# Optimization experiments

Hardware: AMD Instinct MI355X
Metric: run time of the kernel (lower is better)

## Reference

```python
import jax, jax.numpy as jnp
import numpy as np

B, T, R = 512, 4096, 16


def setup_inputs() -> dict:
    key = jax.random.key(0)
    k1, k2, k3 = jax.random.split(key, 3)
    pred = jax.random.normal(k1, (B, T, R), dtype=jnp.float32)
    target = jax.random.normal(k2, (B, T, R), dtype=jnp.float32)
    # replicate_mask marks a contiguous prefix of valid replicates (matches
    # the original `pred[b, :, :n_valid]` slicing). Lengths in [0, R].
    lengths = jax.random.randint(k3, (B,), 0, R + 1)
    replicate_mask = (jnp.arange(R)[None, :] < lengths[:, None]).astype(jnp.float32)
    return {"pred": pred, "target": target, "replicate_mask": replicate_mask}


def _masked_var_unbiased(x, m, n_safe):
    # x: [B,T,R], m: [B,1,R], n_safe: [B,1] (clamped >= 2)
    mean = jnp.sum(x * m, axis=-1, keepdims=True) / n_safe[:, :, None]  # [B,T,1]
    sq = jnp.sum(((x - mean) ** 2) * m, axis=-1)  # [B,T]
    return sq / (n_safe - 1.0)  # unbiased (torch var default ddof=1)


def reference(pred, target, replicate_mask):
    weight = 0.1
    n = jnp.sum(replicate_mask, axis=-1)  # [B]
    n_safe = jnp.maximum(n, 2.0)[:, None]  # avoid div-by-zero; masked out below
    m = replicate_mask[:, None, :]  # [B,1,R]
    pred_var = _masked_var_unbiased(pred, m, n_safe)      # [B,T]
    target_var = _masked_var_unbiased(target, m, n_safe)  # [B,T]
    mse = jnp.mean((pred_var - target_var) ** 2, axis=-1)  # [B]
    valid = n > 1.0
    n_multi = jnp.sum(valid.astype(jnp.float32))
    total = jnp.sum(jnp.where(valid, mse, 0.0))
    loss = jnp.where(n_multi > 0, total / jnp.maximum(n_multi, 1.0), 0.0)
    return weight * loss
```

## Files before the change

### kernel.cpp

```cpp
#include <hip/hip_runtime.h>

#define B_DIM 512
#define T_DIM 4096
#define NSLOT 256
#define BLOCKS 16384
#define THREADS 256
#define NWAVE (THREADS / 64)
#define ITER 2

__device__ __forceinline__ float hsum4(float4 v) { return (v.x + v.y) + (v.z + v.w); }

__device__ __forceinline__ float mdot(float4 x, float4 m) {
    return (x.x * m.x + x.y * m.y) + (x.z * m.z + x.w * m.w);
}

__device__ __forceinline__ float mdot2(float4 x, float4 m) {
    return (x.x * x.x * m.x + x.y * x.y * m.y) + (x.z * x.z * m.z + x.w * x.w * m.w);
}

__device__ __forceinline__ float qsum(float v) {
    int t = __builtin_amdgcn_update_dpp(0, __float_as_int(v), 0xB1, 0xF, 0xF, true);
    v += __int_as_float(t);
    t = __builtin_amdgcn_update_dpp(0, __float_as_int(v), 0x4E, 0xF, 0xF, true);
    v += __int_as_float(t);
    return v;
}

__device__ __forceinline__ void stage16(const float4* g, float4* l) {
    __builtin_amdgcn_global_load_lds((const __attribute__((address_space(1))) void*)g,
                                     (__attribute__((address_space(3))) void*)l, 16, 0, 0);
}

__global__ __launch_bounds__(THREADS) void rcl_main(
    const float4* __restrict__ pred4, const float4* __restrict__ targ4,
    const float4* __restrict__ mask4, double* __restrict__ slots)
{
    __shared__ float4 buf[2][NWAVE][ITER][64];

    const int tid = threadIdx.x;
    const int w = tid >> 6;
    const int lane = tid & 63;
    const int tid0 = blockIdx.x * THREADS + tid;

    float4 mv[ITER];
#pragma unroll
    for (int i = 0; i < ITER; i++) {
        const int g = tid0 + i * (BLOCKS * THREADS);
        mv[i] = mask4[((g >> 14) << 2) + (g & 3)];
    }

    float nval[ITER];
#pragma unroll
    for (int i = 0; i < ITER; i++) {
        const int g = tid0 + i * (BLOCKS * THREADS);
        nval[i] = qsum(hsum4(mv[i]));
        if (nval[i] > 1.0f) {
            stage16(&pred4[g], &buf[0][w][i][0]);
            stage16(&targ4[g], &buf[1][w][i][0]);
        }
    }

    __syncthreads();

    float csum = 0.0f;
#pragma unroll
    for (int i = 0; i < ITER; i++) {
        if (nval[i] > 1.0f) {
            const float4 m = mv[i];
            const float4 p = buf[0][w][i][lane];
            const float4 q = buf[1][w][i][lane];
            float sp  = qsum(mdot(p, m));
            float sp2 = qsum(mdot2(p, m));
            float sq  = qsum(mdot(q, m));
            float sq2 = qsum(mdot2(q, m));

            const float n = nval[i];
            float inv = 1.0f / (n * (n - 1.0f));
            float d = ((n * sp2 - sp * sp) - (n * sq2 - sq * sq)) * inv;
            csum += d * d * 0.25f;
        }
    }

    for (int off = 32; off > 0; off >>= 1)
        csum += __shfl_down(csum, off, 64);

    __shared__ float partial[NWAVE];
    if (lane == 0) partial[w] = csum;
    __syncthreads();
    if (tid == 0) {
        float s = (partial[0] + partial[1]) + (partial[2] + partial[3]);
        atomicAdd(&slots[blockIdx.x & (NSLOT - 1)], (double)s);
    }
}

__global__ __launch_bounds__(256) void rcl_final(
    const double* __restrict__ slots, const float4* __restrict__ mask4,
    float* __restrict__ out)
{
    __shared__ double dred[256];
    __shared__ float fred[256];
    const int t = threadIdx.x;

    double tot = slots[t];

    float cnt = 0.0f;
    for (int bb = t; bb < B_DIM; bb += 256) {
        const float4* mp = mask4 + (bb << 2);
        float nn = (hsum4(mp[0]) + hsum4(mp[1])) + (hsum4(mp[2]) + hsum4(mp[3]));
        cnt += (nn > 1.0f) ? 1.0f : 0.0f;
    }

    dred[t] = tot;
    fred[t] = cnt;
    __syncthreads();
    for (int s = 128; s > 0; s >>= 1) {
        if (t < s) { dred[t] += dred[t + s]; fred[t] += fred[t + s]; }
        __syncthreads();
    }
    if (t == 0) {
        double nm = (double)fred[0];
        out[0] = (nm > 0.0) ? (float)(0.1 * (dred[0] / ((double)T_DIM * nm))) : 0.0f;
    }
}

extern "C" void kernel_launch(void* const* d_in, const int* in_sizes, int n_in,
                              void* d_out, int out_size, void* d_ws, size_t ws_size,
                              hipStream_t stream) {
    const float4* pred4 = (const float4*)d_in[0];
    const float4* targ4 = (const float4*)d_in[1];
    const float4* mask4 = (const float4*)d_in[2];
    float* out = (float*)d_out;

    double* slots = (double*)d_ws;

    hipMemsetAsync(d_ws, 0, NSLOT * sizeof(double), stream);
    rcl_main<<<BLOCKS, THREADS, 0, stream>>>(pred4, targ4, mask4, slots);
    rcl_final<<<1, 256, 0, stream>>>(slots, mask4, out);
}
```

Before: 270.6 us.

## Assign each block to one batch row and load directly with early exit

Each block now covers 2048 float4 rows that all belong to a single batch element, with 8 iterations per thread and plain global loads instead of global_load_lds staging through LDS plus a barrier. The mask count and reciprocal are computed once per block, and blocks for batches with n<=1 return before issuing any loads. The grid shrinks fourfold and launch bounds request 4 blocks per CU. The cost is less parallelism per block and reliance on the compiler's unrolling to keep enough loads in flight.

```diff
diff --git a/kernel.cpp b/kernel.cpp
--- a/kernel.cpp
+++ b/kernel.cpp
@@ -3,10 +3,10 @@
 #define B_DIM 512
 #define T_DIM 4096
 #define NSLOT 256
-#define BLOCKS 16384
 #define THREADS 256
-#define NWAVE (THREADS / 64)
-#define ITER 2
+#define ITER 8
+#define QROWS (B_DIM * T_DIM * 4)
+#define BLOCKS (QROWS / (THREADS * ITER))
 
 __device__ __forceinline__ float hsum4(float4 v) { return (v.x + v.y) + (v.z + v.w); }
 
@@ -26,65 +26,40 @@
     return v;
 }
 
-__device__ __forceinline__ void stage16(const float4* g, float4* l) {
-    __builtin_amdgcn_global_load_lds((const __attribute__((address_space(1))) void*)g,
-                                     (__attribute__((address_space(3))) void*)l, 16, 0, 0);
-}
-
-__global__ __launch_bounds__(THREADS) void rcl_main(
+__global__ __launch_bounds__(THREADS, 4) void rcl_main(
     const float4* __restrict__ pred4, const float4* __restrict__ targ4,
     const float4* __restrict__ mask4, double* __restrict__ slots)
 {
-    __shared__ float4 buf[2][NWAVE][ITER][64];
+    const int tid  = threadIdx.x;
+    const int b    = blockIdx.x >> 3;
+    const int base = blockIdx.x * (THREADS * ITER);
 
-    const int tid = threadIdx.x;
-    const int w = tid >> 6;
-    const int lane = tid & 63;
-    const int tid0 = blockIdx.x * THREADS + tid;
+    const float4 mv = mask4[(b << 2) + (tid & 3)];
+    const float n = qsum(hsum4(mv));
+    if (n <= 1.0f) return;
 
-    float4 mv[ITER];
-#pragma unroll
-    for (int i = 0; i < ITER; i++) {
-        const int g = tid0 + i * (BLOCKS * THREADS);
-        mv[i] = mask4[((g >> 14) << 2) + (g & 3)];
-    }
-
-    float nval[ITER];
-#pragma unroll
-    for (int i = 0; i < ITER; i++) {
-        const int g = tid0 + i * (BLOCKS * THREADS);
-        nval[i] = qsum(hsum4(mv[i]));
-        if (nval[i] > 1.0f) {
-            stage16(&pred4[g], &buf[0][w][i][0]);
-            stage16(&targ4[g], &buf[1][w][i][0]);
-        }
-    }
-
-    __syncthreads();
+    const float inv = 1.0f / (n * (n - 1.0f));
 
     float csum = 0.0f;
 #pragma unroll
     for (int i = 0; i < ITER; i++) {
-        if (nval[i] > 1.0f) {
-            const float4 m = mv[i];
-            const float4 p = buf[0][w][i][lane];
-            const float4 q = buf[1][w][i][lane];
-            float sp  = qsum(mdot(p, m));
-            float sp2 = qsum(mdot2(p, m));
-            float sq  = qsum(mdot(q, m));
-            float sq2 = qsum(mdot2(q, m));
-
-            const float n = nval[i];
-            float inv = 1.0f / (n * (n - 1.0f));
-            float d = ((n * sp2 - sp * sp) - (n * sq2 - sq * sq)) * inv;
-            csum += d * d * 0.25f;
-        }
+        const int g = base + i * THREADS + tid;
+        const float4 p = pred4[g];
+        const float4 q = targ4[g];
+        float sp  = qsum(mdot(p, mv));
+        float sp2 = qsum(mdot2(p, mv));
+        float sq  = qsum(mdot(q, mv));
+        float sq2 = qsum(mdot2(q, mv));
+        float d = ((n * sp2 - sp * sp) - (n * sq2 - sq * sq)) * inv;
+        csum += d * d * 0.25f;
     }
 
     for (int off = 32; off > 0; off >>= 1)
         csum += __shfl_down(csum, off, 64);
 
-    __shared__ float partial[NWAVE];
+    __shared__ float partial[THREADS / 64];
+    const int w = tid >> 6;
+    const int lane = tid & 63;
     if (lane == 0) partial[w] = csum;
     __syncthreads();
     if (tid == 0) {
```

Measured after the change: 274.2 us. No clear change (+1.3%).
